# Kernel optimization log

Measured on AMD Instinct MI355X. Metric: run time of the kernel, lower is better.

Reference implementation:

```python
import jax, jax.numpy as jnp
import numpy as np

DIM = 1024
H = 16
DH = DIM // H
SCALE = DH ** -0.5
EPS = 1e-5


def _linear_params(key, fan_in, fan_out):
    k1, k2 = jax.random.split(key)
    bound = 1.0 / np.sqrt(fan_in)
    w = jax.random.uniform(k1, (fan_out, fan_in), jnp.float32, -bound, bound)
    b = jax.random.uniform(k2, (fan_out,), jnp.float32, -bound, bound)
    return w, b


def setup_inputs() -> dict:
    key = jax.random.key(0)
    ks = jax.random.split(key, 16)
    M, K, S_txt, S_img = 32, 128, 1024, 768
    inp = {
        'entity_text': jax.random.normal(ks[0], (M, K, DIM), jnp.float32),
        'entity_image': jax.random.normal(ks[1], (M, K, DIM), jnp.float32),
        'img_feat': jax.random.normal(ks[2], (M, S_img, DIM), jnp.float32),
        'txt_feat': jax.random.normal(ks[3], (M, S_txt, DIM), jnp.float32),
    }
    img_mask = jax.random.randint(ks[4], (M, S_img), 0, 2, jnp.int32)
    txt_mask = jax.random.randint(ks[5], (M, S_txt), 0, 2, jnp.int32)
    # guarantee at least one valid kv token per row (avoids all -inf rows)
    inp['img_mask'] = img_mask.at[:, 0].set(1)
    inp['txt_mask'] = txt_mask.at[:, 0].set(1)
    names = ['wq_t', 'wk_t', 'wv_t', 'wo_t', 'wq_i', 'wk_i', 'wv_i', 'wo_i']
    for i, n in enumerate(names):
        w, b = _linear_params(ks[6 + i], DIM, DIM)
        inp[n] = w
        inp['b' + n[1:]] = b
    inp['g_t'] = jnp.ones((DIM,), jnp.float32)
    inp['beta_t'] = jnp.zeros((DIM,), jnp.float32)
    inp['g_i'] = jnp.ones((DIM,), jnp.float32)
    inp['beta_i'] = jnp.zeros((DIM,), jnp.float32)
    return inp


def _attend(wq, bq, wk, bk, wv, bv, wo, bo, queries, kv, kv_mask):
    M, K, D = queries.shape
    S = kv.shape[1]
    Q = (queries @ wq.T + bq).reshape(M, K, H, DH)
    Kt = (kv @ wk.T + bk).reshape(M, S, H, DH)
    V = (kv @ wv.T + bv).reshape(M, S, H, DH)
    attn = jnp.einsum('mkhd,mshd->mhks', Q, Kt) * SCALE  # [M,H,K,S]
    attn = jnp.where(kv_mask[:, None, None, :] > 0, attn, -jnp.inf)
    attn = jax.nn.softmax(attn, axis=-1)
    attn = jnp.nan_to_num(attn, nan=0.0)  # dropout=eval mode (identity)
    out = jnp.einsum('mhks,mshd->mkhd', attn, V).reshape(M, K, D)
    return out @ wo.T + bo


def _layernorm(x, g, b):
    mu = jnp.mean(x, axis=-1, keepdims=True)
    var = jnp.mean(jnp.square(x - mu), axis=-1, keepdims=True)
    return (x - mu) * jax.lax.rsqrt(var + EPS) * g + b


def reference(entity_text, entity_image, img_feat, txt_feat, img_mask, txt_mask,
              wq_t, bq_t, wk_t, bk_t, wv_t, bv_t, wo_t, bo_t,
              wq_i, bq_i, wk_i, bk_i, wv_i, bv_i, wo_i, bo_i,
              g_t, beta_t, g_i, beta_i):
    out_t = _attend(wq_t, bq_t, wk_t, bk_t, wv_t, bv_t, wo_t, bo_t,
                    entity_text, txt_feat, txt_mask)
    out_i = _attend(wq_i, bq_i, wk_i, bk_i, wv_i, bv_i, wo_i, bo_i,
                    entity_image, img_feat, img_mask)
    et = _layernorm(entity_text + out_t, g_t, beta_t)
    ei = _layernorm(entity_image + out_i, g_i, beta_i)
    return (et, ei)
```

## Files before the change

### kernel.cpp

```cpp
#include <hip/hip_runtime.h>
#include <stdint.h>

typedef unsigned short u16;
typedef __attribute__((ext_vector_type(8))) short short8;
typedef __attribute__((ext_vector_type(4))) float f32x4;

#define SWZ(r) (((r) & 7) << 4)
#define SCALE 0.125f

__device__ __forceinline__ u16 f2bf(float f) {
  unsigned int x = __float_as_uint(f);
  x += 0x7fffu + ((x >> 16) & 1u);
  return (u16)(x >> 16);
}

__device__ __forceinline__ unsigned int cvtpk_bf16(float lo, float hi) {
  unsigned int r;
  asm("v_cvt_pk_bf16_f32 %0, %1, %2" : "=v"(r) : "v"(lo), "v"(hi));
  return r;
}

__device__ __forceinline__ f32x4 mfma16(short8 a, short8 b, f32x4 c) {
  return __builtin_amdgcn_mfma_f32_16x16x32_bf16(a, b, c, 0, 0, 0);
}

__device__ __forceinline__ void gload_lds16(const u16* g, u16* l) {
  __builtin_amdgcn_global_load_lds(
      (const __attribute__((address_space(1))) unsigned int*)g,
      (__attribute__((address_space(3))) unsigned int*)l, 16, 0, 0);
}

__device__ __forceinline__ int xcd_swz(int bid, int nwg) {
  int cpx = nwg >> 3;
  return (bid & 7) * cpx + (bid >> 3);
}

__global__ __launch_bounds__(256) void cvt_w_kernel(
    const float* __restrict__ s0, const float* __restrict__ s1,
    const float* __restrict__ s2, const float* __restrict__ s3,
    u16* __restrict__ dst) {
  int bx = blockIdx.x;
  int mi = bx >> 9;
  const float* s = s0;
  if (mi == 1) s = s1;
  else if (mi == 2) s = s2;
  else if (mi == 3) s = s3;
  size_t idx = (size_t)((bx & 511) * 256 + threadIdx.x) * 8;
  float4 a = *(const float4*)(s + idx);
  float4 b = *(const float4*)(s + idx + 4);
  uint4 u;
  u.x = cvtpk_bf16(a.x, a.y);
  u.y = cvtpk_bf16(a.z, a.w);
  u.z = cvtpk_bf16(b.x, b.y);
  u.w = cvtpk_bf16(b.z, b.w);
  *(uint4*)(dst + (size_t)mi * 1048576 + idx) = u;
}

__global__ __launch_bounds__(256) void cvt_a_kernel(
    const float* __restrict__ src, u16* __restrict__ dst, int n8) {
  int i = blockIdx.x * 256 + threadIdx.x;
  int stride = gridDim.x * 256;
  for (; i < n8; i += stride) {
    size_t idx = (size_t)i * 8;
    float4 a = *(const float4*)(src + idx);
    float4 b = *(const float4*)(src + idx + 4);
    uint4 u;
    u.x = cvtpk_bf16(a.x, a.y);
    u.y = cvtpk_bf16(a.z, a.w);
    u.z = cvtpk_bf16(b.x, b.y);
    u.w = cvtpk_bf16(b.z, b.w);
    *(uint4*)(dst + idx) = u;
  }
}

template <bool A_F32, bool OUT_F32>
__global__ __launch_bounds__(256, 2) void gemm_bias_kernel(
    const void* __restrict__ Av, const u16* __restrict__ B,
    const float* __restrict__ bias0, const float* __restrict__ bias1,
    void* __restrict__ Cv, int ldc) {
  __shared__ __attribute__((aligned(16))) u16 As[128 * 64];
  __shared__ __attribute__((aligned(16))) u16 Bs[128 * 64];
  const int tid = threadIdx.x;
  const int lane = tid & 63;
  const int w = tid >> 6;
  const int wr = w >> 1, wc = w & 1;
  const int l15 = lane & 15, lg = lane >> 4;

  const int nwg = gridDim.x * gridDim.y;
  const int lid = xcd_swz(blockIdx.y * gridDim.x + blockIdx.x, nwg);
  const int bx = lid % gridDim.x;
  const int by = lid / gridDim.x;
  const int brow = by * 128;
  const int bcol = bx * 128;

  f32x4 acc[4][4] = {};

  for (int k0 = 0; k0 < 1024; k0 += 64) {
#pragma unroll
    for (int p = 0; p < 4; ++p) {
      int flat = p * 256 + tid;
      int row = flat >> 3;
      int cb = (flat & 7) * 16;
      int scb = cb ^ SWZ(row);
      const u16* src = B + (size_t)(bcol + row) * 1024 + k0 + (scb >> 1);
      gload_lds16(src, Bs + (size_t)flat * 8);
    }
    if constexpr (A_F32) {
      const float* Af = (const float*)Av;
#pragma unroll
      for (int p = 0; p < 4; ++p) {
        int flat = p * 256 + tid;
        int row = flat >> 3;
        int c8 = flat & 7;
        const float* src = Af + (size_t)(brow + row) * 1024 + k0 + c8 * 8;
        float4 v0 = ((const float4*)src)[0];
        float4 v1 = ((const float4*)src)[1];
        uint4 u;
        u.x = cvtpk_bf16(v0.x, v0.y);
        u.y = cvtpk_bf16(v0.z, v0.w);
        u.z = cvtpk_bf16(v1.x, v1.y);
        u.w = cvtpk_bf16(v1.z, v1.w);
        *(uint4*)((char*)As + row * 128 + ((c8 * 16) ^ SWZ(row))) = u;
      }
    } else {
      const u16* Ab = (const u16*)Av;
#pragma unroll
      for (int p = 0; p < 4; ++p) {
        int flat = p * 256 + tid;
        int row = flat >> 3;
        int cb = (flat & 7) * 16;
        int scb = cb ^ SWZ(row);
        const u16* src = Ab + (size_t)(brow + row) * 1024 + k0 + (scb >> 1);
        gload_lds16(src, As + (size_t)flat * 8);
      }
    }
    __syncthreads();

    short8 af[4][2], bfr[4][2];
#pragma unroll
    for (int i = 0; i < 4; ++i) {
#pragma unroll
      for (int kk = 0; kk < 2; ++kk) {
        int ar = wr * 64 + i * 16 + l15;
        af[i][kk] = *(const short8*)((const char*)As + ar * 128 +
                                     ((kk * 64 + lg * 16) ^ SWZ(ar)));
        int br = wc * 64 + i * 16 + l15;
        bfr[i][kk] = *(const short8*)((const char*)Bs + br * 128 +
                                      ((kk * 64 + lg * 16) ^ SWZ(br)));
      }
    }
#pragma unroll
    for (int i = 0; i < 4; ++i)
#pragma unroll
      for (int j = 0; j < 4; ++j)
#pragma unroll
        for (int kk = 0; kk < 2; ++kk)
          acc[i][j] = mfma16(af[i][kk], bfr[j][kk], acc[i][j]);
    __syncthreads();
  }

#pragma unroll
  for (int j = 0; j < 4; ++j) {
    int col = bcol + wc * 64 + j * 16 + l15;
    const float* bp = (col < 1024) ? bias0 : bias1;
    float bv = bp[col & 1023];
#pragma unroll
    for (int i = 0; i < 4; ++i) {
      int row0 = brow + wr * 64 + i * 16 + lg * 4;
#pragma unroll
      for (int r = 0; r < 4; ++r) {
        float v = acc[i][j][r] + bv;
        if constexpr (OUT_F32)
          ((float*)Cv)[(size_t)(row0 + r) * ldc + col] = v;
        else
          ((u16*)Cv)[(size_t)(row0 + r) * ldc + col] = f2bf(v);
      }
    }
  }
}

__global__ __launch_bounds__(256, 2) void attn_mfma_kernel(
    const u16* __restrict__ Q, const u16* __restrict__ KV,
    const int* __restrict__ mask, u16* __restrict__ AO, int S, int mbase) {
  __shared__ __attribute__((aligned(16))) u16 Ks[64 * 64];
  __shared__ __attribute__((aligned(16))) u16 Vt[64 * 64];
  __shared__ __attribute__((aligned(16))) u16 Ps[4 * 32 * 64];
  __shared__ float mb[64];

  const int tid = threadIdx.x;
  const int lane = tid & 63;
  const int w = tid >> 6;
  const int lid = xcd_swz(blockIdx.x, gridDim.x);
  const int ml = lid >> 4;
  const int h = lid & 15;
  const int mg = mbase + ml;
  const int l15 = lane & 15, lg = lane >> 4;

  short8 qf[2][2];
#pragma unroll
  for (int qb = 0; qb < 2; ++qb)
#pragma unroll
    for (int kk = 0; kk < 2; ++kk)
      qf[qb][kk] = *(const short8*)(Q + (size_t)(mg * 128 + w * 32 + qb * 16 + l15) * 1024 +
                                    h * 64 + kk * 32 + lg * 8);

  float mrun[2][4], lrun[2][4];
  f32x4 oacc[2][4] = {};
#pragma unroll
  for (int qb = 0; qb < 2; ++qb)
#pragma unroll
    for (int r = 0; r < 4; ++r) {
      mrun[qb][r] = -1e30f;
      lrun[qb][r] = 0.0f;
    }

  const size_t kvbase = (size_t)ml * S * 2048 + h * 64;

  for (int st = 0; st < S; st += 64) {
    if (tid < 64)
      mb[tid] = (mask[(size_t)mg * S + st + tid] > 0) ? 0.0f : -1e30f;
#pragma unroll
    for (int p = 0; p < 2; ++p) {
      int flat = p * 256 + tid;
      int row = flat >> 3;
      int c = flat & 7;
      short8 v = *(const short8*)(KV + kvbase + (size_t)(st + row) * 2048 + c * 8);
      *(short8*)((char*)Ks + row * 128 + ((c * 16) ^ SWZ(row))) = v;
    }
#pragma unroll
    for (int p = 0; p < 2; ++p) {
      int flat = p * 256 + tid;
      int srow = flat >> 3;
      int c = flat & 7;
      short8 v = *(const short8*)(KV + kvbase + 1024 + (size_t)(st + srow) * 2048 + c * 8);
#pragma unroll
      for (int j = 0; j < 8; ++j) {
        int dr = c * 8 + j;
        *(u16*)((char*)Vt + dr * 128 + ((srow * 2) ^ SWZ(dr))) = (u16)v[j];
      }
    }
    __syncthreads();

    short8 kf[4][2];
#pragma unroll
    for (int sb = 0; sb < 4; ++sb)
#pragma unroll
      for (int kk = 0; kk < 2; ++kk) {
        int row = sb * 16 + l15;
        kf[sb][kk] = *(const short8*)((const char*)Ks + row * 128 +
                                      ((kk * 64 + lg * 16) ^ SWZ(row)));
      }
    f32x4 sc[2][4] = {};
#pragma unroll
    for (int qb = 0; qb < 2; ++qb)
#pragma unroll
      for (int sb = 0; sb < 4; ++sb)
#pragma unroll
        for (int kk = 0; kk < 2; ++kk)
          sc[qb][sb] = mfma16(qf[qb][kk], kf[sb][kk], sc[qb][sb]);

    float mbv[4];
#pragma unroll
    for (int sb = 0; sb < 4; ++sb) mbv[sb] = mb[sb * 16 + l15];

#pragma unroll
    for (int qb = 0; qb < 2; ++qb) {
#pragma unroll
      for (int r = 0; r < 4; ++r) {
        float s0 = sc[qb][0][r] * SCALE + mbv[0];
        float s1 = sc[qb][1][r] * SCALE + mbv[1];
        float s2 = sc[qb][2][r] * SCALE + mbv[2];
        float s3 = sc[qb][3][r] * SCALE + mbv[3];
        float t = fmaxf(fmaxf(s0, s1), fmaxf(s2, s3));
        for (int d = 1; d < 16; d <<= 1) t = fmaxf(t, __shfl_xor(t, d));
        float mnew = fmaxf(mrun[qb][r], t);
        float resc = __expf(mrun[qb][r] - mnew);
        float p0 = __expf(s0 - mnew);
        float p1 = __expf(s1 - mnew);
        float p2 = __expf(s2 - mnew);
        float p3 = __expf(s3 - mnew);
        float rs = p0 + p1 + p2 + p3;
        for (int d = 1; d < 16; d <<= 1) rs += __shfl_xor(rs, d);
        lrun[qb][r] = lrun[qb][r] * resc + rs;
        mrun[qb][r] = mnew;
#pragma unroll
        for (int db = 0; db < 4; ++db) oacc[qb][db][r] *= resc;
        int row = qb * 16 + lg * 4 + r;
        char* pbase = (char*)Ps + (w * 32 + row) * 128;
        int colb = 2 * l15;
        *(u16*)(pbase + ((0 * 32 + colb) ^ SWZ(row))) = f2bf(p0);
        *(u16*)(pbase + ((1 * 32 + colb) ^ SWZ(row))) = f2bf(p1);
        *(u16*)(pbase + ((2 * 32 + colb) ^ SWZ(row))) = f2bf(p2);
        *(u16*)(pbase + ((3 * 32 + colb) ^ SWZ(row))) = f2bf(p3);
      }
    }
    __syncthreads();

    short8 pf[2][2], vf[4][2];
#pragma unroll
    for (int qb = 0; qb < 2; ++qb)
#pragma unroll
      for (int kk = 0; kk < 2; ++kk) {
        int row = qb * 16 + l15;
        pf[qb][kk] = *(const short8*)((const char*)Ps + (w * 32 + row) * 128 +
                                      ((kk * 64 + lg * 16) ^ SWZ(row)));
      }
#pragma unroll
    for (int db = 0; db < 4; ++db)
#pragma unroll
      for (int kk = 0; kk < 2; ++kk) {
        int row = db * 16 + l15;
        vf[db][kk] = *(const short8*)((const char*)Vt + row * 128 +
                                      ((kk * 64 + lg * 16) ^ SWZ(row)));
      }
#pragma unroll
    for (int qb = 0; qb < 2; ++qb)
#pragma unroll
      for (int db = 0; db < 4; ++db)
#pragma unroll
        for (int kk = 0; kk < 2; ++kk)
          oacc[qb][db] = mfma16(pf[qb][kk], vf[db][kk], oacc[qb][db]);
    __syncthreads();
  }

#pragma unroll
  for (int qb = 0; qb < 2; ++qb)
#pragma unroll
    for (int db = 0; db < 4; ++db)
#pragma unroll
      for (int r = 0; r < 4; ++r) {
        int grow = mg * 128 + w * 32 + qb * 16 + lg * 4 + r;
        int gcol = h * 64 + db * 16 + l15;
        float v = oacc[qb][db][r] / lrun[qb][r];
        AO[(size_t)grow * 1024 + gcol] = f2bf(v);
      }
}

__global__ __launch_bounds__(256) void ln_kernel(
    const float* __restrict__ X, const float* __restrict__ O,
    const float* __restrict__ g, const float* __restrict__ b,
    float* __restrict__ out) {
  int row = blockIdx.x;
  int tid = threadIdx.x;
  const float* xr = X + (size_t)row * 1024;
  const float* orr = O + (size_t)row * 1024;
  float4 xv = *(const float4*)(xr + tid * 4);
  float4 ov = *(const float4*)(orr + tid * 4);
  float v0 = xv.x + ov.x, v1 = xv.y + ov.y, v2 = xv.z + ov.z, v3 = xv.w + ov.w;
  float s = v0 + v1 + v2 + v3;
  float s2 = v0 * v0 + v1 * v1 + v2 * v2 + v3 * v3;
  for (int d = 1; d < 64; d <<= 1) {
    s += __shfl_xor(s, d);
    s2 += __shfl_xor(s2, d);
  }
  __shared__ float ps[4], ps2[4];
  int w = tid >> 6;
  if ((tid & 63) == 0) {
    ps[w] = s;
    ps2[w] = s2;
  }
  __syncthreads();
  s = ps[0] + ps[1] + ps[2] + ps[3];
  s2 = ps2[0] + ps2[1] + ps2[2] + ps2[3];
  float mu = s * (1.0f / 1024.0f);
  float var = s2 * (1.0f / 1024.0f) - mu * mu;
  float rstd = rsqrtf(var + 1e-5f);
  float4 gv = *(const float4*)(g + tid * 4);
  float4 bv = *(const float4*)(b + tid * 4);
  float4 ou;
  ou.x = (v0 - mu) * rstd * gv.x + bv.x;
  ou.y = (v1 - mu) * rstd * gv.y + bv.y;
  ou.z = (v2 - mu) * rstd * gv.z + bv.z;
  ou.w = (v3 - mu) * rstd * gv.w + bv.w;
  *(float4*)(out + (size_t)row * 1024 + tid * 4) = ou;
}

extern "C" void kernel_launch(void* const* d_in, const int* in_sizes, int n_in,
                              void* d_out, int out_size, void* d_ws, size_t ws_size,
                              hipStream_t stream) {
  const float* ent_t = (const float*)d_in[0];
  const float* ent_i = (const float*)d_in[1];
  const float* img_feat = (const float*)d_in[2];
  const float* txt_feat = (const float*)d_in[3];
  const int* img_mask = (const int*)d_in[4];
  const int* txt_mask = (const int*)d_in[5];
  const float* W[8];
  const float* Bv[8];
  for (int i = 0; i < 8; ++i) {
    W[i] = (const float*)d_in[6 + 2 * i];
    Bv[i] = (const float*)d_in[7 + 2 * i];
  }
  const float* g_t = (const float*)d_in[22];
  const float* beta_t = (const float*)d_in[23];
  const float* g_i = (const float*)d_in[24];
  const float* beta_i = (const float*)d_in[25];
  float* out = (float*)d_out;

  int nc = 0;
  size_t Xt = 0;
  for (int t = 1; t <= 4; t <<= 1) {
    size_t x = (134217728ull) / t;
    if ((32ull << 20) + x + x / 2 <= ws_size) { nc = t; Xt = x; break; }
  }

  char* ws = (char*)d_ws;
  u16* Wbf = (u16*)ws;
  u16* Qbf = (u16*)(ws + (8ull << 20));
  u16* AObf = (u16*)(ws + (16ull << 20));

  if (nc > 0) {
    u16* entbf = (u16*)(ws + (24ull << 20));
    u16* KVc = (u16*)(ws + (32ull << 20));
    u16* featbf = (u16*)(ws + (32ull << 20) + Xt);
    float* Of32 = (float*)(ws + (32ull << 20));
    const int mpc = 32 / nc;

    for (int mod = 0; mod < 2; ++mod) {
      const float* ent = mod ? ent_i : ent_t;
      const float* feat = mod ? img_feat : txt_feat;
      const int* msk = mod ? img_mask : txt_mask;
      int S = mod ? 768 : 1024;

      cvt_w_kernel<<<2048, 256, 0, stream>>>(W[mod * 4 + 0], W[mod * 4 + 1],
                                             W[mod * 4 + 2], W[mod * 4 + 3], Wbf);
      cvt_a_kernel<<<2048, 256, 0, stream>>>(ent, entbf, 4096 * 128);

      const u16* wq = Wbf + 0ull * 1048576;
      const u16* wkv = Wbf + 1ull * 1048576;
      const u16* wo = Wbf + 3ull * 1048576;
      const float* bq = Bv[mod * 4 + 0];
      const float* bk = Bv[mod * 4 + 1];
      const float* bvv = Bv[mod * 4 + 2];
      const float* bo = Bv[mod * 4 + 3];

      gemm_bias_kernel<false, false><<<dim3(8, 32), 256, 0, stream>>>(
          entbf, wq, bq, bq, Qbf, 1024);

      int crows = mpc * S;
      for (int c = 0; c < nc; ++c) {
        const float* featc = feat + (size_t)c * mpc * S * 1024;
        cvt_a_kernel<<<2048, 256, 0, stream>>>(featc, featbf, crows * 128);
        gemm_bias_kernel<false, false><<<dim3(16, crows / 128), 256, 0, stream>>>(
            featbf, wkv, bk, bvv, KVc, 2048);
        attn_mfma_kernel<<<mpc * 16, 256, 0, stream>>>(Qbf, KVc, msk, AObf, S, c * mpc);
      }

      gemm_bias_kernel<false, true><<<dim3(8, 32), 256, 0, stream>>>(
          AObf, wo, bo, bo, Of32, 1024);
      ln_kernel<<<4096, 256, 0, stream>>>(ent, Of32,
                                          mod ? g_i : g_t, mod ? beta_i : beta_t,
                                          out + (size_t)mod * 4194304);
    }
  } else {
    int ncf = 4;
    if (ws_size >= (152ull << 20)) ncf = 1;
    else if (ws_size >= (88ull << 20)) ncf = 2;
    u16* KVc = (u16*)(ws + (24ull << 20));
    float* Of32 = (float*)(ws + (24ull << 20));
    const int mpc = 32 / ncf;

    for (int mod = 0; mod < 2; ++mod) {
      const float* ent = mod ? ent_i : ent_t;
      const float* feat = mod ? img_feat : txt_feat;
      const int* msk = mod ? img_mask : txt_mask;
      int S = mod ? 768 : 1024;

      cvt_w_kernel<<<2048, 256, 0, stream>>>(W[mod * 4 + 0], W[mod * 4 + 1],
                                             W[mod * 4 + 2], W[mod * 4 + 3], Wbf);

      const u16* wq = Wbf + 0ull * 1048576;
      const u16* wkv = Wbf + 1ull * 1048576;
      const u16* wo = Wbf + 3ull * 1048576;
      const float* bq = Bv[mod * 4 + 0];
      const float* bk = Bv[mod * 4 + 1];
      const float* bvv = Bv[mod * 4 + 2];
      const float* bo = Bv[mod * 4 + 3];

      gemm_bias_kernel<true, false><<<dim3(8, 32), 256, 0, stream>>>(
          ent, wq, bq, bq, Qbf, 1024);

      int crows = mpc * S;
      for (int c = 0; c < ncf; ++c) {
        const float* featc = feat + (size_t)c * mpc * S * 1024;
        gemm_bias_kernel<true, false><<<dim3(16, crows / 128), 256, 0, stream>>>(
            featc, wkv, bk, bvv, KVc, 2048);
        attn_mfma_kernel<<<mpc * 16, 256, 0, stream>>>(Qbf, KVc, msk, AObf, S, c * mpc);
      }

      gemm_bias_kernel<false, true><<<dim3(8, 32), 256, 0, stream>>>(
          AObf, wo, bo, bo, Of32, 1024);
      ln_kernel<<<4096, 256, 0, stream>>>(ent, Of32,
                                          mod ? g_i : g_t, mod ? beta_i : beta_t,
                                          out + (size_t)mod * 4194304);
    }
  }
}
```

Baseline: 537.6 us.

## Merge conversion launches and fuse Q projection into first KV GEMM launch

Replaces the separate weight, entity and first feature-chunk fp32-to-bf16 conversion kernels with one grid-stride kernel. The Q projection GEMM and the first chunk's KV projection GEMM now run in a single launch, with block ranges dispatched to each problem. This cuts launch count and lets the small Q GEMM fill the GPU alongside the larger KV GEMM, at the cost of branchier conversion code.

```diff
diff --git a/kernel.cpp b/kernel.cpp
--- a/kernel.cpp
+++ b/kernel.cpp
@@ -35,41 +35,138 @@
   return (bid & 7) * cpx + (bid >> 3);
 }
 
-__global__ __launch_bounds__(256) void cvt_w_kernel(
-    const float* __restrict__ s0, const float* __restrict__ s1,
-    const float* __restrict__ s2, const float* __restrict__ s3,
-    u16* __restrict__ dst) {
-  int bx = blockIdx.x;
-  int mi = bx >> 9;
-  const float* s = s0;
-  if (mi == 1) s = s1;
-  else if (mi == 2) s = s2;
-  else if (mi == 3) s = s3;
-  size_t idx = (size_t)((bx & 511) * 256 + threadIdx.x) * 8;
-  float4 a = *(const float4*)(s + idx);
-  float4 b = *(const float4*)(s + idx + 4);
+__device__ __forceinline__ void cvt8(const float* src, u16* dst) {
+  float4 a = *(const float4*)src;
+  float4 b = *(const float4*)(src + 4);
   uint4 u;
   u.x = cvtpk_bf16(a.x, a.y);
   u.y = cvtpk_bf16(a.z, a.w);
   u.z = cvtpk_bf16(b.x, b.y);
   u.w = cvtpk_bf16(b.z, b.w);
-  *(uint4*)(dst + (size_t)mi * 1048576 + idx) = u;
+  *(uint4*)dst = u;
+}
+
+__global__ __launch_bounds__(256) void cvt_all_kernel(
+    const float* __restrict__ w0, const float* __restrict__ w1,
+    const float* __restrict__ w2, const float* __restrict__ w3,
+    const float* __restrict__ ent, const float* __restrict__ feat,
+    u16* __restrict__ Wbf, u16* __restrict__ entbf, u16* __restrict__ featbf,
+    int nE8, int nF8) {
+  const int nW8 = 524288;
+  int total = nW8 + nE8 + nF8;
+  int i = blockIdx.x * 256 + threadIdx.x;
+  int stride = gridDim.x * 256;
+  for (; i < total; i += stride) {
+    if (i < nW8) {
+      int mi = i >> 17;
+      const float* s = (mi == 0) ? w0 : (mi == 1) ? w1 : (mi == 2) ? w2 : w3;
+      size_t off = (size_t)(i & 131071) * 8;
+      cvt8(s + off, Wbf + (size_t)mi * 1048576 + off);
+    } else if (i < nW8 + nE8) {
+      size_t off = (size_t)(i - nW8) * 8;
+      cvt8(ent + off, entbf + off);
+    } else {
+      size_t off = (size_t)(i - nW8 - nE8) * 8;
+      cvt8(feat + off, featbf + off);
+    }
+  }
 }
 
 __global__ __launch_bounds__(256) void cvt_a_kernel(
     const float* __restrict__ src, u16* __restrict__ dst, int n8) {
   int i = blockIdx.x * 256 + threadIdx.x;
   int stride = gridDim.x * 256;
-  for (; i < n8; i += stride) {
-    size_t idx = (size_t)i * 8;
-    float4 a = *(const float4*)(src + idx);
-    float4 b = *(const float4*)(src + idx + 4);
-    uint4 u;
-    u.x = cvtpk_bf16(a.x, a.y);
-    u.y = cvtpk_bf16(a.z, a.w);
-    u.z = cvtpk_bf16(b.x, b.y);
-    u.w = cvtpk_bf16(b.z, b.w);
-    *(uint4*)(dst + idx) = u;
+  for (; i < n8; i += stride) cvt8(src + (size_t)i * 8, dst + (size_t)i * 8);
+}
+
+__device__ __forceinline__ void gemm_core_bf16(
+    const u16* __restrict__ A, const u16* __restrict__ B,
+    const float* __restrict__ bias0, const float* __restrict__ bias1,
+    u16* __restrict__ C, int ldc, int bx, int by, u16* As, u16* Bs) {
+  const int tid = threadIdx.x;
+  const int lane = tid & 63;
+  const int w = tid >> 6;
+  const int wr = w >> 1, wc = w & 1;
+  const int l15 = lane & 15, lg = lane >> 4;
+  const int brow = by * 128;
+  const int bcol = bx * 128;
+
+  f32x4 acc[4][4] = {};
+
+  for (int k0 = 0; k0 < 1024; k0 += 64) {
+#pragma unroll
+    for (int p = 0; p < 4; ++p) {
+      int flat = p * 256 + tid;
+      int row = flat >> 3;
+      int cb = (flat & 7) * 16;
+      int scb = cb ^ SWZ(row);
+      gload_lds16(B + (size_t)(bcol + row) * 1024 + k0 + (scb >> 1),
+                  Bs + (size_t)flat * 8);
+    }
+#pragma unroll
+    for (int p = 0; p < 4; ++p) {
+      int flat = p * 256 + tid;
+      int row = flat >> 3;
+      int cb = (flat & 7) * 16;
+      int scb = cb ^ SWZ(row);
+      gload_lds16(A + (size_t)(brow + row) * 1024 + k0 + (scb >> 1),
+                  As + (size_t)flat * 8);
+    }
+    __syncthreads();
+
+    short8 af[4][2], bfr[4][2];
+#pragma unroll
+    for (int i = 0; i < 4; ++i) {
+#pragma unroll
+      for (int kk = 0; kk < 2; ++kk) {
+        int ar = wr * 64 + i * 16 + l15;
+        af[i][kk] = *(const short8*)((const char*)As + ar * 128 +
+                                     ((kk * 64 + lg * 16) ^ SWZ(ar)));
+        int br = wc * 64 + i * 16 + l15;
+        bfr[i][kk] = *(const short8*)((const char*)Bs + br * 128 +
+                                      ((kk * 64 + lg * 16) ^ SWZ(br)));
+      }
+    }
+#pragma unroll
+    for (int i = 0; i < 4; ++i)
+#pragma unroll
+      for (int j = 0; j < 4; ++j)
+#pragma unroll
+        for (int kk = 0; kk < 2; ++kk)
+          acc[i][j] = mfma16(af[i][kk], bfr[j][kk], acc[i][j]);
+    __syncthreads();
+  }
+
+#pragma unroll
+  for (int j = 0; j < 4; ++j) {
+    int col = bcol + wc * 64 + j * 16 + l15;
+    const float* bp = (col < 1024) ? bias0 : bias1;
+    float bv = bp[col & 1023];
+#pragma unroll
+    for (int i = 0; i < 4; ++i) {
+      int row0 = brow + wr * 64 + i * 16 + lg * 4;
+#pragma unroll
+      for (int r = 0; r < 4; ++r)
+        C[(size_t)(row0 + r) * ldc + col] = f2bf(acc[i][j][r] + bv);
+    }
+  }
+}
+
+__global__ __launch_bounds__(256, 2) void qkv_gemm_kernel(
+    const u16* __restrict__ A0, const u16* __restrict__ B0,
+    const float* __restrict__ bq, u16* __restrict__ C0, int gx0, int nwg0,
+    const u16* __restrict__ A1, const u16* __restrict__ B1,
+    const float* __restrict__ bk, const float* __restrict__ bv,
+    u16* __restrict__ C1, int gx1, int nwg1) {
+  __shared__ __attribute__((aligned(16))) u16 As[128 * 64];
+  __shared__ __attribute__((aligned(16))) u16 Bs[128 * 64];
+  int bid = blockIdx.x;
+  if (bid < nwg0) {
+    int lid = xcd_swz(bid, nwg0);
+    gemm_core_bf16(A0, B0, bq, bq, C0, 1024, lid % gx0, lid / gx0, As, Bs);
+  } else {
+    int lid = xcd_swz(bid - nwg0, nwg1);
+    gemm_core_bf16(A1, B1, bk, bv, C1, 2048, lid % gx1, lid / gx1, As, Bs);
   }
 }
 
@@ -102,8 +199,8 @@
       int row = flat >> 3;
       int cb = (flat & 7) * 16;
       int scb = cb ^ SWZ(row);
-      const u16* src = B + (size_t)(bcol + row) * 1024 + k0 + (scb >> 1);
-      gload_lds16(src, Bs + (size_t)flat * 8);
+      gload_lds16(B + (size_t)(bcol + row) * 1024 + k0 + (scb >> 1),
+                  Bs + (size_t)flat * 8);
     }
     if constexpr (A_F32) {
       const float* Af = (const float*)Av;
@@ -130,8 +227,8 @@
         int row = flat >> 3;
         int cb = (flat & 7) * 16;
         int scb = cb ^ SWZ(row);
-        const u16* src = Ab + (size_t)(brow + row) * 1024 + k0 + (scb >> 1);
-        gload_lds16(src, As + (size_t)flat * 8);
+        gload_lds16(Ab + (size_t)(brow + row) * 1024 + k0 + (scb >> 1),
+                    As + (size_t)flat * 8);
       }
     }
     __syncthreads();
@@ -399,7 +496,7 @@
   int nc = 0;
   size_t Xt = 0;
   for (int t = 1; t <= 4; t <<= 1) {
-    size_t x = (134217728ull) / t;
+    size_t x = 134217728ull / t;
     if ((32ull << 20) + x + x / 2 <= ws_size) { nc = t; Xt = x; break; }
   }
 
@@ -420,10 +517,7 @@
       const float* feat = mod ? img_feat : txt_feat;
       const int* msk = mod ? img_mask : txt_mask;
       int S = mod ? 768 : 1024;
-
-      cvt_w_kernel<<<2048, 256, 0, stream>>>(W[mod * 4 + 0], W[mod * 4 + 1],
-                                             W[mod * 4 + 2], W[mod * 4 + 3], Wbf);
-      cvt_a_kernel<<<2048, 256, 0, stream>>>(ent, entbf, 4096 * 128);
+      int crows = mpc * S;
 
       const u16* wq = Wbf + 0ull * 1048576;
       const u16* wkv = Wbf + 1ull * 1048576;
@@ -433,15 +527,20 @@
       const float* bvv = Bv[mod * 4 + 2];
       const float* bo = Bv[mod * 4 + 3];
 
-      gemm_bias_kernel<false, false><<<dim3(8, 32), 256, 0, stream>>>(
-          entbf, wq, bq, bq, Qbf, 1024);
-
-      int crows = mpc * S;
+      cvt_all_kernel<<<2048, 256, 0, stream>>>(
+          W[mod * 4 + 0], W[mod * 4 + 1], W[mod * 4 + 2], W[mod * 4 + 3],
+          ent, feat, Wbf, entbf, featbf, 4096 * 128, crows * 128);
+
       for (int c = 0; c < nc; ++c) {
-        const float* featc = feat + (size_t)c * mpc * S * 1024;
-        cvt_a_kernel<<<2048, 256, 0, stream>>>(featc, featbf, crows * 128);
-        gemm_bias_kernel<false, false><<<dim3(16, crows / 128), 256, 0, stream>>>(
-            featbf, wkv, bk, bvv, KVc, 2048);
+        if (c > 0) {
+          const float* featc = feat + (size_t)c * mpc * S * 1024;
+          cvt_a_kernel<<<2048, 256, 0, stream>>>(featc, featbf, crows * 128);
+        }
+        int nwg0 = (c == 0) ? 256 : 0;
+        int nwg1 = 16 * (crows / 128);
+        qkv_gemm_kernel<<<nwg0 + nwg1, 256, 0, stream>>>(
+            entbf, wq, bq, Qbf, 8, nwg0,
+            featbf, wkv, bk, bvv, KVc, 16, nwg1);
         attn_mfma_kernel<<<mpc * 16, 256, 0, stream>>>(Qbf, KVc, msk, AObf, S, c * mpc);
       }
 
@@ -465,8 +564,9 @@
       const int* msk = mod ? img_mask : txt_mask;
       int S = mod ? 768 : 1024;
 
-      cvt_w_kernel<<<2048, 256, 0, stream>>>(W[mod * 4 + 0], W[mod * 4 + 1],
-                                             W[mod * 4 + 2], W[mod * 4 + 3], Wbf);
+      cvt_all_kernel<<<2048, 256, 0, stream>>>(
+          W[mod * 4 + 0], W[mod * 4 + 1], W[mod * 4 + 2], W[mod * 4 + 3],
+          ent, ent, Wbf, Qbf , Qbf, 0, 0);
 
       const u16* wq = Wbf + 0ull * 1048576;
       const u16* wkv = Wbf + 1ull * 1048576;
```

New measurement: 525.0 us. 1.02x faster.
